# Optimization experiments

Hardware: AMD Instinct MI355X
Metric: run time of the kernel (lower is better)

## Reference

```python
import jax, jax.numpy as jnp
import numpy as np

B, V, T, F, H = 32, 16, 64, 64, 512
NBINS = 36  # 360 / delta (delta_cog = delta_rb = 10)
OUT = 4     # output_size


def setup_inputs() -> dict:
    key = jax.random.key(0)
    ks = jax.random.split(key, 12)
    s = 1.0 / np.sqrt(H)
    return {
        'sequence': jax.random.normal(ks[0], (B, V, T, F), jnp.float32),
        'dist_matrix': jax.random.uniform(ks[1], (B, V, T, V), jnp.float32),
        'rb_matrix': jax.random.randint(ks[2], (B, V, T, V), 0, NBINS).astype(jnp.int32),
        'cog_matrix': jax.random.randint(ks[3], (B, V, T, V), 0, NBINS).astype(jnp.int32),
        'seq_mask': jnp.ones((B, V, T), jnp.float32),
        'maxval': jax.random.uniform(ks[4], (B, F), jnp.float32) + 1.0,
        'minval': jax.random.uniform(ks[5], (B, F), jnp.float32),
        # per-vessel LSTMCell params (PyTorch gate order i,f,g,o stacked along 4H)
        'W_ih': jax.random.normal(ks[6], (V, 4 * H, F), jnp.float32) * s,
        'W_hh': jax.random.normal(ks[7], (V, 4 * H, H), jnp.float32) * s,
        'b_ih': jnp.zeros((V, 4 * H), jnp.float32),
        'b_hh': jnp.zeros((V, 4 * H), jnp.float32),
        # hardwired attention domain table [360/delta_cog, 360/delta_rb]
        'domain': jax.random.normal(ks[8], (NBINS, NBINS), jnp.float32),
        # per-vessel softAttention linear (2H -> H)
        'soft_W': jax.random.normal(ks[9], (V, H, 2 * H), jnp.float32) * s,
        'soft_b': jnp.zeros((V, H), jnp.float32),
        # shared output linear (H -> F)
        'out_W': jax.random.normal(ks[10], (F, H), jnp.float32) * s,
        'out_b': jnp.zeros((F,), jnp.float32),
    }


def _forward(sequence, dist_matrix, rb_matrix, cog_matrix, seq_mask, maxval, minval,
             W_ih, W_hh, b_ih, b_hh, domain, soft_W, soft_b, out_W, out_b):
    B_, V_, T_, F_ = sequence.shape
    H_ = W_hh.shape[-1]

    def hardwired(h, r, d, m, cg):
        # h: [B,V,H]; r,d,cg: [B,V,V]; m: [B,V]
        mul1 = m[:, :, None] * m[:, None, :]
        mul2 = domain[cg, r]
        w = jax.nn.relu(mul2 - d) * mul1
        w = w / jax.lax.stop_gradient(jnp.max(w))  # torch: weights /= weights.data.max()
        return jnp.einsum('bvw,bwh->bvh', w, h)

    def lstm_step(x, h, c):
        # vectorized over V independent LSTMCells
        g = (jnp.einsum('bvf,vgf->bvg', x, W_ih)
             + jnp.einsum('bvh,vgh->bvg', h, W_hh) + b_ih + b_hh)
        i, f, gg, o = jnp.split(g, 4, axis=-1)
        c_new = jax.nn.sigmoid(f) * c + jax.nn.sigmoid(i) * jnp.tanh(gg)
        h_new = jax.nn.sigmoid(o) * jnp.tanh(c_new)
        return h_new, c_new

    h0 = jnp.zeros((B_, V_, H_), sequence.dtype)
    c0 = jnp.zeros((B_, V_, H_), sequence.dtype)
    xs = (jnp.moveaxis(sequence, 2, 0), jnp.moveaxis(rb_matrix, 2, 0),
          jnp.moveaxis(dist_matrix, 2, 0), jnp.moveaxis(seq_mask, 2, 0),
          jnp.moveaxis(cog_matrix, 2, 0))

    def enc_step(carry, xt):
        h, c = carry
        x, r, d, m, cg = xt
        wh = hardwired(h, r, d, m, cg)
        h, c = lstm_step(x, wh, c)
        return (h, c), h

    (h, c), enc = jax.lax.scan(enc_step, (h0, c0), xs)
    enc = jnp.moveaxis(enc, 0, 2)  # encodedInput [B,V,T,H]

    # decoder, prediction step i=0 (prediction_length=1)
    wh = hardwired(h, rb_matrix[:, :, -1], dist_matrix[:, :, -1],
                   seq_mask[:, :, -1], cog_matrix[:, :, -1])
    # get_previous_sequence: denormalize under no_grad
    prev = jax.lax.stop_gradient(
        sequence[:, :, -1] * (maxval - minval)[:, None, :] + minval[:, None, :])
    h, c = lstm_step(prev, wh, c)

    # per-vessel softAttention
    score = jnp.einsum('bvth,bvh->bvt', enc, h)
    alpha = jax.nn.softmax(score * seq_mask, axis=-1)
    ctx = jnp.einsum('bvt,bvth->bvh', alpha, enc)
    # faithful to torch.stack((ctx, h)).view(B, 2H) memory-reinterpret per vessel
    z = jnp.moveaxis(jnp.stack([ctx, h], axis=0), 2, 0).reshape(V_, B_, 2 * H_)
    h = jnp.moveaxis(
        jnp.tanh(jnp.einsum('vbk,vhk->vbh', z, soft_W) + soft_b[:, None, :]), 0, 1)

    out = jax.nn.relu(jnp.einsum('bvh,fh->bvf', h, out_W) + out_b)
    return out[:, :, None, :OUT]  # [B, V, prediction_length=1, output_size]


def reference(sequence, dist_matrix, rb_matrix, cog_matrix, seq_mask, maxval, minval,
              W_ih, W_hh, b_ih, b_hh, domain, soft_W, soft_b, out_W, out_b,
              maxVessels=V):
    return _forward(sequence, dist_matrix, rb_matrix, cog_matrix, seq_mask,
                    maxval, minval, W_ih, W_hh, b_ih, b_hh, domain,
                    soft_W, soft_b, out_W, out_b)
```

## Files before the change

kernel.cpp:

```cpp
#include <hip/hip_runtime.h>
#include <math.h>

#define B 32
#define V 16
#define T 64
#define F 64
#define H 512
#define NB 36
#define G4H 2048

typedef unsigned short u16;
typedef unsigned long long ull;
typedef __attribute__((ext_vector_type(8))) short bf16x8;
typedef __attribute__((ext_vector_type(4))) float f32x4;

#define OFF_H0     0
#define OFF_H1     262144
#define OFF_C      524288
#define OFF_CNT    786432
#define OFF_WALL   819200
#define OFF_CTX    819200
#define OFF_HSOFT  1081344
#define OFF_WMAX   1343488
#define OFF_WHSTG  1343552
#define OFF_SEQSTG 1605696
#define OFF_WSTG   2670656
#define OFF_ENC    12107840

#define WHP 262144
#define WLDS_BYTES 147456

__device__ __forceinline__ float sigmoidf_(float x) { return 1.0f / (1.0f + __expf(-x)); }

__device__ __forceinline__ u16 f2bf(float f) {
    union { float f; unsigned u; } x; x.f = f;
    unsigned r = x.u + 0x7FFF + ((x.u >> 16) & 1);
    return (u16)(r >> 16);
}
__device__ __forceinline__ float bf2f(u16 u) {
    union { unsigned i; float f; } x; x.i = ((unsigned)u) << 16;
    return x.f;
}
__device__ __forceinline__ f32x4 mfma16(bf16x8 a, bf16x8 b, f32x4 c) {
    return __builtin_amdgcn_mfma_f32_16x16x32_bf16(a, b, c, 0, 0, 0);
}
__device__ __forceinline__ bf16x8 mk_bf16x8(ull lo, ull hi) {
    union { ull u[2]; bf16x8 v; } x; x.u[0] = lo; x.u[1] = hi; return x.v;
}
__device__ __forceinline__ bf16x8 mk_bf16x8q(uint4 q) {
    union { uint4 q; bf16x8 v; } x; x.q = q; return x.v;
}

__device__ __forceinline__ ull ld_agent(const ull* p) {
    return __hip_atomic_load((ull*)p, __ATOMIC_RELAXED, __HIP_MEMORY_SCOPE_AGENT);
}
__device__ __forceinline__ void st_agent(ull* p, ull x) {
    __hip_atomic_store(p, x, __ATOMIC_RELAXED, __HIP_MEMORY_SCOPE_AGENT);
}
__device__ __forceinline__ void st_agent_f(float* p, float x) {
    __hip_atomic_store(p, x, __ATOMIC_RELAXED, __HIP_MEMORY_SCOPE_AGENT);
}
__device__ __forceinline__ void st_agent_u32(unsigned* p, unsigned x) {
    __hip_atomic_store(p, x, __ATOMIC_RELAXED, __HIP_MEMORY_SCOPE_AGENT);
}
__device__ __forceinline__ unsigned ld_agent_u32(const unsigned* p) {
    return __hip_atomic_load((unsigned*)p, __ATOMIC_RELAXED, __HIP_MEMORY_SCOPE_AGENT);
}

#define NZB 3200
#define NHW 64
#define NWC 256
#define NSS 1040
__global__ __launch_bounds__(256) void k_prep(
    float* __restrict__ ws,
    const float* __restrict__ dist, const int* __restrict__ rb,
    const int* __restrict__ cog, const float* __restrict__ mask,
    const float* __restrict__ domain, float* __restrict__ w_all,
    float* __restrict__ wmax_all,
    const float* __restrict__ W_ih, const float* __restrict__ W_hh,
    u16* __restrict__ Wstg,
    const float* __restrict__ seq, const float* __restrict__ maxval,
    const float* __restrict__ minval, u16* __restrict__ seqstg) {
    __shared__ float red[256];
    __shared__ float tile[128 * 36];
    int bid = blockIdx.x;
    int tid = threadIdx.x;

    if (bid < NZB) {
        ws[bid * 256 + tid] = 0.0f;
        return;
    }
    if (bid < NZB + NHW) {
        int t = bid - NZB;
        float lmax = 0.0f;
        for (int idx = tid; idx < B * V * V; idx += 256) {
            int b = idx >> 8;
            int rem = idx & 255;
            int i = rem >> 4, j = rem & 15;
            int base = ((b * V + i) * T + t) * V + j;
            float val = domain[cog[base] * NB + rb[base]] - dist[base];
            val = val > 0.0f ? val : 0.0f;
            val *= mask[(b * V + i) * T + t] * mask[(b * V + j) * T + t];
            w_all[t * (B * V * V) + idx] = val;
            lmax = fmaxf(lmax, val);
        }
        red[tid] = lmax;
        __syncthreads();
        for (int s = 128; s > 0; s >>= 1) {
            if (tid < s) red[tid] = fmaxf(red[tid], red[tid + s]);
            __syncthreads();
        }
        if (tid == 0) wmax_all[t] = red[0];
        return;
    }
    if (bid < NZB + NHW + NWC) {
        int idx = bid - (NZB + NHW);
        int v = idx >> 4, hk = idx & 15;
        int lr = tid >> 1, half = tid & 1;
        int lg = lr >> 5, rloc = lr & 31;
        int srcrow = v * G4H + lg * 512 + hk * 32 + rloc;
        for (int ks = 0; ks < 18; ++ks) {
            const float* srcp = (ks < 2)
                ? &W_ih[srcrow * F + ks * 32 + half * 16]
                : &W_hh[srcrow * H + (ks * 32 - 64) + half * 16];
            float4 x0 = *(const float4*)srcp;
            float4 x1 = *(const float4*)(srcp + 4);
            float4 x2 = *(const float4*)(srcp + 8);
            float4 x3 = *(const float4*)(srcp + 12);
            __syncthreads();
            float* dst = &tile[lr * 36 + half * 16];
            *(float4*)(dst + 0) = x0;
            *(float4*)(dst + 4) = x1;
            *(float4*)(dst + 8) = x2;
            *(float4*)(dst + 12) = x3;
            __syncthreads();
#pragma unroll
            for (int s = 0; s < 2; ++s) {
                int slot = tid + s * 256;
                int nt = slot >> 6, lane = slot & 63;
                int g = nt >> 1, hh = nt & 1;
                int ldsrow = g * 32 + hh * 16 + (lane & 15);
                int kloc = (lane >> 4) << 3;
                float4 y0 = *(const float4*)&tile[ldsrow * 36 + kloc];
                float4 y1 = *(const float4*)&tile[ldsrow * 36 + kloc + 4];
                union { u16 u[8]; uint4 q; } pk;
                pk.u[0] = f2bf(y0.x); pk.u[1] = f2bf(y0.y);
                pk.u[2] = f2bf(y0.z); pk.u[3] = f2bf(y0.w);
                pk.u[4] = f2bf(y1.x); pk.u[5] = f2bf(y1.y);
                pk.u[6] = f2bf(y1.z); pk.u[7] = f2bf(y1.w);
                *(uint4*)&Wstg[(size_t)((((v * 16 + hk) * 18 + ks) * 8 + nt) * 64 + lane) * 8] = pk.q;
            }
        }
        return;
    }
    {
        int idx = bid - (NZB + NHW + NWC);
        int v = idx / 65, t = idx % 65;
        int mt = tid >> 7, ks = (tid >> 6) & 1, lane = tid & 63;
        int b = mt * 16 + (lane & 15);
        int f = ks * 32 + ((lane >> 4) << 3);
        union { u16 u[8]; uint4 q; } pk;
        if (t < T) {
            const float* sp = &seq[((b * V + v) * T + t) * F + f];
            float4 x0 = *(const float4*)sp, x1 = *(const float4*)(sp + 4);
            pk.u[0] = f2bf(x0.x); pk.u[1] = f2bf(x0.y); pk.u[2] = f2bf(x0.z); pk.u[3] = f2bf(x0.w);
            pk.u[4] = f2bf(x1.x); pk.u[5] = f2bf(x1.y); pk.u[6] = f2bf(x1.z); pk.u[7] = f2bf(x1.w);
        } else {
            const float* sp = &seq[((b * V + v) * T + (T - 1)) * F + f];
            float4 x0 = *(const float4*)sp, x1 = *(const float4*)(sp + 4);
            float4 mx0 = *(const float4*)&maxval[b * F + f], mx1 = *(const float4*)&maxval[b * F + f + 4];
            float4 mn0 = *(const float4*)&minval[b * F + f], mn1 = *(const float4*)&minval[b * F + f + 4];
            pk.u[0] = f2bf(x0.x * (mx0.x - mn0.x) + mn0.x);
            pk.u[1] = f2bf(x0.y * (mx0.y - mn0.y) + mn0.y);
            pk.u[2] = f2bf(x0.z * (mx0.z - mn0.z) + mn0.z);
            pk.u[3] = f2bf(x0.w * (mx0.w - mn0.w) + mn0.w);
            pk.u[4] = f2bf(x1.x * (mx1.x - mn1.x) + mn1.x);
            pk.u[5] = f2bf(x1.y * (mx1.y - mn1.y) + mn1.y);
            pk.u[6] = f2bf(x1.z * (mx1.z - mn1.z) + mn1.z);
            pk.u[7] = f2bf(x1.w * (mx1.w - mn1.w) + mn1.w);
        }
        *(uint4*)&seqstg[(((size_t)(t * 16 + v)) * 4 + mt * 2 + ks) * 512 + lane * 8] = pk.q;
    }
}

__global__ __launch_bounds__(256) void k_recur(
    const u16* __restrict__ seqstg, const u16* __restrict__ Wstg,
    const float* __restrict__ w_all, const float* __restrict__ wmax_all,
    const float* __restrict__ b_ih, const float* __restrict__ b_hh,
    float* __restrict__ h0buf, float* __restrict__ h1buf,
    float* __restrict__ c, u16* __restrict__ enc, u16* __restrict__ whstg,
    unsigned* __restrict__ bar) {
    extern __shared__ u16 Wlds[];

    int bid = blockIdx.x;
    int v = bid & 15, hk = bid >> 4;
    int tid = threadIdx.x;

    {
        const uint4* wsrc = (const uint4*)(Wstg + (size_t)((v * 16 + hk) * 18) * 4096);
        uint4* wdst = (uint4*)Wlds;
        for (int i = tid; i < 9216; i += 256) wdst[i] = wsrc[i];
    }

    int lane = tid & 63, wvi = tid >> 6;
    int mtw = wvi & 1, hh = wvi >> 1;
    int col = hk * 32 + hh * 16 + (lane & 15);
    int q4 = (lane >> 4) << 2;
    float bi = b_ih[v * G4H + col] + b_hh[v * G4H + col];
    float bf_ = b_ih[v * G4H + H + col] + b_hh[v * G4H + H + col];
    float bg_ = b_ih[v * G4H + 2 * H + col] + b_hh[v * G4H + 2 * H + col];
    float bo = b_ih[v * G4H + 3 * H + col] + b_hh[v * G4H + 3 * H + col];

    unsigned* aslot = bar + (v * 16 + hk) * 16;
    unsigned* bslot = bar + (256 + hk * 16 + v) * 16;
    unsigned* apoll = bar + (v * 16 + (tid & 15)) * 16;
    unsigned* bpoll = bar + (256 + hk * 16 + (tid & 15)) * 16;

    int a_b = tid >> 3;
    int a_cq = tid & 7;
    const int wh_idx = ((((v * 2 + (a_b >> 4)) * 16 + hk) * 64 +
                         (((a_cq >> 1) << 4) + (a_b & 15))) * 8 + (a_cq & 1) * 4);

    __syncthreads();

    for (int t = 0; t <= T; ++t) {
        int par = t & 1;
        int tm = t < T ? t : (T - 1);
        const float* hin = (t & 1) ? h0buf : h1buf;
        float* hout = (t & 1) ? h1buf : h0buf;

        uint4 s0 = *(const uint4*)&seqstg[(((size_t)(t * 16 + v)) * 4 + mtw * 2 + 0) * 512 + lane * 8];
        uint4 s1 = *(const uint4*)&seqstg[(((size_t)(t * 16 + v)) * 4 + mtw * 2 + 1) * 512 + lane * 8];
        float inv = 1.0f / wmax_all[tm];
        const float* wrow = &w_all[(size_t)tm * (B * V * V) + (a_b * V + v) * V];
        float4 wr0 = *(const float4*)(wrow);
        float4 wr1 = *(const float4*)(wrow + 4);
        float4 wr2 = *(const float4*)(wrow + 8);
        float4 wr3 = *(const float4*)(wrow + 12);
        float cprev[4];
#pragma unroll
        for (int r = 0; r < 4; ++r)
            cprev[r] = c[((mtw * 16 + q4 + r) * V + v) * H + col];

        f32x4 acc[4];
        acc[0][0] = bi;  acc[0][1] = bi;  acc[0][2] = bi;  acc[0][3] = bi;
        acc[1][0] = bf_; acc[1][1] = bf_; acc[1][2] = bf_; acc[1][3] = bf_;
        acc[2][0] = bg_; acc[2][1] = bg_; acc[2][2] = bg_; acc[2][3] = bg_;
        acc[3][0] = bo;  acc[3][1] = bo;  acc[3][2] = bo;  acc[3][3] = bo;
        {
            bf16x8 a0f = mk_bf16x8q(s0);
            bf16x8 a1f = mk_bf16x8q(s1);
#pragma unroll
            for (int g = 0; g < 4; ++g)
                acc[g] = mfma16(a0f, *(const bf16x8*)&Wlds[(0 * 8 + (g * 2 + hh)) * 512 + lane * 8], acc[g]);
#pragma unroll
            for (int g = 0; g < 4; ++g)
                acc[g] = mfma16(a1f, *(const bf16x8*)&Wlds[(1 * 8 + (g * 2 + hh)) * 512 + lane * 8], acc[g]);
        }

        if (t > 0) {
            if (tid < 16) {
                while (ld_agent_u32(bpoll) < (unsigned)t) __builtin_amdgcn_s_sleep(1);
            }
            __syncthreads();
        }

        {
            const ull* hb = (const ull*)&hin[(a_b * V) * H + hk * 32 + a_cq * 4];
            float a0 = 0.f, a1 = 0.f, a2 = 0.f, a3 = 0.f;
            const float wj[16] = {wr0.x, wr0.y, wr0.z, wr0.w, wr1.x, wr1.y, wr1.z, wr1.w,
                                  wr2.x, wr2.y, wr2.z, wr2.w, wr3.x, wr3.y, wr3.z, wr3.w};
#pragma unroll
            for (int j = 0; j < 16; ++j) {
                ull lo = ld_agent(hb + (size_t)j * (H / 2));
                ull hi = ld_agent(hb + (size_t)j * (H / 2) + 1);
                union { ull u; float f[2]; } u0, u1;
                u0.u = lo; u1.u = hi;
                a0 = fmaf(wj[j], u0.f[0], a0);
                a1 = fmaf(wj[j], u0.f[1], a1);
                a2 = fmaf(wj[j], u1.f[0], a2);
                a3 = fmaf(wj[j], u1.f[1], a3);
            }
            union { u16 u[4]; ull q; } pk;
            pk.u[0] = f2bf(a0 * inv); pk.u[1] = f2bf(a1 * inv);
            pk.u[2] = f2bf(a2 * inv); pk.u[3] = f2bf(a3 * inv);
            st_agent((ull*)&whstg[par * WHP + wh_idx], pk.q);
        }
        __syncthreads();
        if (tid == 0) st_agent_u32(aslot, (unsigned)(t + 1));

        if (tid < 16) {
            while (ld_agent_u32(apoll) < (unsigned)(t + 1)) __builtin_amdgcn_s_sleep(1);
        }
        __syncthreads();

        bf16x8 afr[16];
#pragma unroll
        for (int ksw = 0; ksw < 16; ++ksw) {
            const ull* src = (const ull*)&whstg[par * WHP + (((v * 2 + mtw) * 16 + ksw) * 64 + lane) * 8];
            ull lo = ld_agent(src), hi = ld_agent(src + 1);
            afr[ksw] = mk_bf16x8(lo, hi);
        }
#pragma unroll
        for (int ks = 0; ks < 16; ++ks) {
#pragma unroll
            for (int g = 0; g < 4; ++g) {
                bf16x8 wfr = *(const bf16x8*)&Wlds[((ks + 2) * 8 + (g * 2 + hh)) * 512 + lane * 8];
                acc[g] = mfma16(afr[ks], wfr, acc[g]);
            }
        }

        float cnv[4], hnv[4];
#pragma unroll
        for (int r = 0; r < 4; ++r) {
            float gi = acc[0][r];
            float gf = acc[1][r];
            float gg = acc[2][r];
            float go = acc[3][r];
            cnv[r] = sigmoidf_(gf) * cprev[r] + sigmoidf_(gi) * tanhf(gg);
            hnv[r] = sigmoidf_(go) * tanhf(cnv[r]);
            int b = mtw * 16 + q4 + r;
            st_agent_f(&hout[(b * V + v) * H + col], hnv[r]);
        }
        if (t < T) {
            __syncthreads();
            if (tid == 0) st_agent_u32(bslot, (unsigned)(t + 1));
        }

#pragma unroll
        for (int r = 0; r < 4; ++r) {
            int b = mtw * 16 + q4 + r;
            c[(b * V + v) * H + col] = cnv[r];
            if (t < T) enc[((size_t)(b * V + v) * T + t) * H + col] = f2bf(hnv[r]);
        }
    }
}

__global__ __launch_bounds__(256) void k_tail(
    const u16* __restrict__ enc, const float* __restrict__ hfin,
    const float* __restrict__ mask, const float* __restrict__ soft_W,
    const float* __restrict__ soft_b, const float* __restrict__ out_W,
    const float* __restrict__ out_b, float* __restrict__ ctx,
    float* __restrict__ hsoft, float* __restrict__ out,
    unsigned* __restrict__ bar) {
    __shared__ float hs[H];
    __shared__ float scal[2 * T];
    __shared__ float sA[32][36];
    __shared__ float sW2[32][36];

    int bid = blockIdx.x;
    int tid = threadIdx.x;
    int lane = tid & 63, wvi = tid >> 6;

    for (int u = 0; u < 2; ++u) {
        int ab = (bid >> 4) + u * 16;
        int av = bid & 15;
        const u16* encb = enc + ((size_t)(ab * V + av) * T) * H;
        {
            float2 q = *(const float2*)(hfin + (ab * V + av) * H + tid * 2);
            hs[tid * 2] = q.x; hs[tid * 2 + 1] = q.y;
        }
        __syncthreads();
        for (int tt = wvi; tt < T; tt += 4) {
            uint4 x = *(const uint4*)(encb + tt * H + lane * 8);
            union { uint4 q; u16 s[8]; } e; e.q = x;
            const float* hq = &hs[lane * 8];
            float p = bf2f(e.s[0]) * hq[0] + bf2f(e.s[1]) * hq[1]
                    + bf2f(e.s[2]) * hq[2] + bf2f(e.s[3]) * hq[3]
                    + bf2f(e.s[4]) * hq[4] + bf2f(e.s[5]) * hq[5]
                    + bf2f(e.s[6]) * hq[6] + bf2f(e.s[7]) * hq[7];
            for (int off = 32; off; off >>= 1) p += __shfl_down(p, off, 64);
            if (lane == 0) scal[tt] = p;
        }
        __syncthreads();
        if (tid < 64) {
            float m_t = mask[(ab * V + av) * T + tid];
            float s = scal[tid] * m_t;
            float mx = s;
            for (int off = 32; off; off >>= 1) mx = fmaxf(mx, __shfl_xor(mx, off, 64));
            float e = __expf(s - mx);
            float sum = e;
            for (int off = 32; off; off >>= 1) sum += __shfl_xor(sum, off, 64);
            scal[T + tid] = e / sum;
        }
        __syncthreads();
        if (tid < 128) {
            float a0 = 0.f, a1 = 0.f, a2 = 0.f, a3 = 0.f;
            for (int tt = 0; tt < T; ++tt) {
                ull x = *(const ull*)(encb + tt * H + tid * 4);
                union { ull u; u16 s[4]; } q; q.u = x;
                float al = scal[T + tt];
                a0 = fmaf(al, bf2f(q.s[0]), a0);
                a1 = fmaf(al, bf2f(q.s[1]), a1);
                a2 = fmaf(al, bf2f(q.s[2]), a2);
                a3 = fmaf(al, bf2f(q.s[3]), a3);
            }
            float* cp = ctx + (ab * V + av) * H + tid * 4;
            union { float f[2]; ull u; } q0, q1;
            q0.f[0] = a0; q0.f[1] = a1; q1.f[0] = a2; q1.f[1] = a3;
            st_agent((ull*)cp, q0.u);
            st_agent((ull*)cp + 1, q1.u);
        }
        __syncthreads();
    }
    __syncthreads();
    if (tid == 0) st_agent_u32(bar + (768 + bid) * 16, 1u);

    {
        int sv = bid & 15;
        int h0 = (bid >> 4) * 32;
        if (tid < 16) {
            const unsigned* cs = bar + (768 + tid * 16 + sv) * 16;
            while (ld_agent_u32(cs) < 1u) __builtin_amdgcn_s_sleep(1);
        }
        __syncthreads();

        int cg = tid & 31, rg = tid >> 5;
        float* sAf = &sA[0][0];
        float* sWf = &sW2[0][0];
        float accs[4] = {0.f, 0.f, 0.f, 0.f};
        int arow = tid >> 3, akq = tid & 7;
        float4 areg, wreg;
        {
            int k = akq * 4;
            const float* src = (arow < 16) ? ctx : hfin;
            int bsrc = 2 * (arow & 15) + (k >= H ? 1 : 0);
            const float* sp = &src[(bsrc * V + sv) * H + (k & (H - 1))];
            ull l0 = ld_agent((const ull*)sp), l1 = ld_agent((const ull*)sp + 1);
            union { ull u[2]; float4 f; } q; q.u[0] = l0; q.u[1] = l1;
            areg = q.f;
            wreg = *(const float4*)&soft_W[(sv * H + h0 + arow) * (2 * H) + k];
        }
        for (int kc = 0; kc < 2 * H; kc += 32) {
            __syncthreads();
            *(float4*)&sAf[arow * 36 + akq * 4] = areg;
            *(float4*)&sWf[arow * 36 + akq * 4] = wreg;
            __syncthreads();
            if (kc + 32 < 2 * H) {
                int k = kc + 32 + akq * 4;
                const float* src = (arow < 16) ? ctx : hfin;
                int bsrc = 2 * (arow & 15) + (k >= H ? 1 : 0);
                const float* sp = &src[(bsrc * V + sv) * H + (k & (H - 1))];
                ull l0 = ld_agent((const ull*)sp), l1 = ld_agent((const ull*)sp + 1);
                union { ull u[2]; float4 f; } q; q.u[0] = l0; q.u[1] = l1;
                areg = q.f;
                wreg = *(const float4*)&soft_W[(sv * H + h0 + arow) * (2 * H) + kc + 32 + akq * 4];
            }
#pragma unroll
            for (int k4 = 0; k4 < 8; ++k4) {
                float4 wv = *(const float4*)&sWf[cg * 36 + k4 * 4];
                float4 a0 = *(const float4*)&sAf[(rg * 4 + 0) * 36 + k4 * 4];
                float4 a1 = *(const float4*)&sAf[(rg * 4 + 1) * 36 + k4 * 4];
                float4 a2 = *(const float4*)&sAf[(rg * 4 + 2) * 36 + k4 * 4];
                float4 a3 = *(const float4*)&sAf[(rg * 4 + 3) * 36 + k4 * 4];
                accs[0] += a0.x * wv.x + a0.y * wv.y + a0.z * wv.z + a0.w * wv.w;
                accs[1] += a1.x * wv.x + a1.y * wv.y + a1.z * wv.z + a1.w * wv.w;
                accs[2] += a2.x * wv.x + a2.y * wv.y + a2.z * wv.z + a2.w * wv.w;
                accs[3] += a3.x * wv.x + a3.y * wv.y + a3.z * wv.z + a3.w * wv.w;
            }
        }
        float bb = soft_b[sv * H + h0 + cg];
#pragma unroll
        for (int r = 0; r < 4; ++r) {
            int row = rg * 4 + r;
            st_agent_f(&hsoft[(row * V + sv) * H + h0 + cg], tanhf(accs[r] + bb));
        }
    }
    __syncthreads();
    if (tid == 0) st_agent_u32(bar + (1024 + bid) * 16, 1u);

    {
        int ov = bid & 15;
        if (tid < 16) {
            const unsigned* ss = bar + (1024 + tid * 16 + ov) * 16;
            while (ld_agent_u32(ss) < 1u) __builtin_amdgcn_s_sleep(1);
        }
        __syncthreads();
        if (wvi < 2) {
            int ob = (bid >> 4) + wvi * 16;
            const float* hbp = hsoft + (ob * V + ov) * H + lane * 8;
            ull q0 = ld_agent((const ull*)hbp);
            ull q1 = ld_agent((const ull*)hbp + 1);
            ull q2 = ld_agent((const ull*)hbp + 2);
            ull q3 = ld_agent((const ull*)hbp + 3);
            union { ull u[4]; float f[8]; } hv;
            hv.u[0] = q0; hv.u[1] = q1; hv.u[2] = q2; hv.u[3] = q3;
            float p[4] = {0.f, 0.f, 0.f, 0.f};
#pragma unroll
            for (int o = 0; o < 4; ++o) {
                const float* wp = &out_W[o * H + lane * 8];
#pragma unroll
                for (int j = 0; j < 8; ++j) p[o] += hv.f[j] * wp[j];
            }
#pragma unroll
            for (int o = 0; o < 4; ++o) {
                float s = p[o];
                for (int off = 32; off; off >>= 1) s += __shfl_down(s, off, 64);
                if (lane == 0) {
                    float val = s + out_b[o];
                    out[(ob * V + ov) * 4 + o] = val > 0.0f ? val : 0.0f;
                }
            }
        }
    }
}

extern "C" void kernel_launch(void* const* d_in, const int* in_sizes, int n_in,
                              void* d_out, int out_size, void* d_ws, size_t ws_size,
                              hipStream_t stream) {
    const float* seq = (const float*)d_in[0];
    const float* dist = (const float*)d_in[1];
    const int* rb = (const int*)d_in[2];
    const int* cog = (const int*)d_in[3];
    const float* mask = (const float*)d_in[4];
    const float* maxval = (const float*)d_in[5];
    const float* minval = (const float*)d_in[6];
    const float* W_ih = (const float*)d_in[7];
    const float* W_hh = (const float*)d_in[8];
    const float* b_ih = (const float*)d_in[9];
    const float* b_hh = (const float*)d_in[10];
    const float* domain = (const float*)d_in[11];
    const float* soft_W = (const float*)d_in[12];
    const float* soft_b = (const float*)d_in[13];
    const float* out_W = (const float*)d_in[14];
    const float* out_b = (const float*)d_in[15];

    float* ws = (float*)d_ws;
    float* h0buf = ws + OFF_H0;
    float* h1buf = ws + OFF_H1;
    float* c = ws + OFF_C;
    unsigned* bar = (unsigned*)(ws + OFF_CNT);
    float* w_all = ws + OFF_WALL;
    float* ctx = ws + OFF_CTX;
    float* hsoft = ws + OFF_HSOFT;
    float* wmax_all = ws + OFF_WMAX;
    u16* whstg = (u16*)(ws + OFF_WHSTG);
    u16* seqstg = (u16*)(ws + OFF_SEQSTG);
    u16* Wstg = (u16*)(ws + OFF_WSTG);
    u16* enc = (u16*)(ws + OFF_ENC);

    (void)hipFuncSetAttribute((const void*)k_recur,
                              hipFuncAttributeMaxDynamicSharedMemorySize, WLDS_BYTES);

    k_prep<<<NZB + NHW + NWC + NSS, 256, 0, stream>>>(
        ws, dist, rb, cog, mask, domain, w_all, wmax_all,
        W_ih, W_hh, Wstg, seq, maxval, minval, seqstg);

    k_recur<<<256, 256, WLDS_BYTES, stream>>>(seqstg, Wstg, w_all, wmax_all,
                                              b_ih, b_hh, h0buf, h1buf, c, enc,
                                              whstg, bar);

    k_tail<<<256, 256, 0, stream>>>(enc, h0buf, mask, soft_W, soft_b,
                                    out_W, out_b, ctx, hsoft,
                                    (float*)d_out, bar);
}
```

Measured before the change: 710.0 us.

## Convert LSTM weights to bf16 directly into LDS inside the recurrent kernel

The prep kernel no longer converts W_ih/W_hh into a global bf16 staging buffer. Each recurrent block now reads fp32 weights from global memory, converts them to bf16 and writes them straight into its LDS tile. Zeroing of h1 and c moves from the prep kernel into the recurrent blocks, so the prep kernel only zeros the counter region. The barrier counter is shifted by one so every block publishes readiness after its own init. This removes a global write-and-reload round trip and most of the zeroing blocks. The cost is slower uncoalesced fp32 loads at the start of the recurrent kernel, and the cross-block barrier protocol changes.

```diff
diff --git a/kernel.cpp b/kernel.cpp
--- a/kernel.cpp
+++ b/kernel.cpp
@@ -24,7 +24,6 @@
 #define OFF_WMAX   1343488
 #define OFF_WHSTG  1343552
 #define OFF_SEQSTG 1605696
-#define OFF_WSTG   2670656
 #define OFF_ENC    12107840
 
 #define WHP 262144
@@ -67,9 +66,8 @@
     return __hip_atomic_load((unsigned*)p, __ATOMIC_RELAXED, __HIP_MEMORY_SCOPE_AGENT);
 }
 
-#define NZB 3200
+#define NZB 80
 #define NHW 64
-#define NWC 256
 #define NSS 1040
 __global__ __launch_bounds__(256) void k_prep(
     float* __restrict__ ws,
@@ -77,17 +75,14 @@
     const int* __restrict__ cog, const float* __restrict__ mask,
     const float* __restrict__ domain, float* __restrict__ w_all,
     float* __restrict__ wmax_all,
-    const float* __restrict__ W_ih, const float* __restrict__ W_hh,
-    u16* __restrict__ Wstg,
     const float* __restrict__ seq, const float* __restrict__ maxval,
     const float* __restrict__ minval, u16* __restrict__ seqstg) {
     __shared__ float red[256];
-    __shared__ float tile[128 * 36];
     int bid = blockIdx.x;
     int tid = threadIdx.x;
 
     if (bid < NZB) {
-        ws[bid * 256 + tid] = 0.0f;
+        ws[OFF_CNT + bid * 256 + tid] = 0.0f;
         return;
     }
     if (bid < NZB + NHW) {
@@ -113,48 +108,8 @@
         if (tid == 0) wmax_all[t] = red[0];
         return;
     }
-    if (bid < NZB + NHW + NWC) {
+    {
         int idx = bid - (NZB + NHW);
-        int v = idx >> 4, hk = idx & 15;
-        int lr = tid >> 1, half = tid & 1;
-        int lg = lr >> 5, rloc = lr & 31;
-        int srcrow = v * G4H + lg * 512 + hk * 32 + rloc;
-        for (int ks = 0; ks < 18; ++ks) {
-            const float* srcp = (ks < 2)
-                ? &W_ih[srcrow * F + ks * 32 + half * 16]
-                : &W_hh[srcrow * H + (ks * 32 - 64) + half * 16];
-            float4 x0 = *(const float4*)srcp;
-            float4 x1 = *(const float4*)(srcp + 4);
-            float4 x2 = *(const float4*)(srcp + 8);
-            float4 x3 = *(const float4*)(srcp + 12);
-            __syncthreads();
-            float* dst = &tile[lr * 36 + half * 16];
-            *(float4*)(dst + 0) = x0;
-            *(float4*)(dst + 4) = x1;
-            *(float4*)(dst + 8) = x2;
-            *(float4*)(dst + 12) = x3;
-            __syncthreads();
-#pragma unroll
-            for (int s = 0; s < 2; ++s) {
-                int slot = tid + s * 256;
-                int nt = slot >> 6, lane = slot & 63;
-                int g = nt >> 1, hh = nt & 1;
-                int ldsrow = g * 32 + hh * 16 + (lane & 15);
-                int kloc = (lane >> 4) << 3;
-                float4 y0 = *(const float4*)&tile[ldsrow * 36 + kloc];
-                float4 y1 = *(const float4*)&tile[ldsrow * 36 + kloc + 4];
-                union { u16 u[8]; uint4 q; } pk;
-                pk.u[0] = f2bf(y0.x); pk.u[1] = f2bf(y0.y);
-                pk.u[2] = f2bf(y0.z); pk.u[3] = f2bf(y0.w);
-                pk.u[4] = f2bf(y1.x); pk.u[5] = f2bf(y1.y);
-                pk.u[6] = f2bf(y1.z); pk.u[7] = f2bf(y1.w);
-                *(uint4*)&Wstg[(size_t)((((v * 16 + hk) * 18 + ks) * 8 + nt) * 64 + lane) * 8] = pk.q;
-            }
-        }
-        return;
-    }
-    {
-        int idx = bid - (NZB + NHW + NWC);
         int v = idx / 65, t = idx % 65;
         int mt = tid >> 7, ks = (tid >> 6) & 1, lane = tid & 63;
         int b = mt * 16 + (lane & 15);
@@ -184,7 +139,8 @@
 }
 
 __global__ __launch_bounds__(256) void k_recur(
-    const u16* __restrict__ seqstg, const u16* __restrict__ Wstg,
+    const u16* __restrict__ seqstg,
+    const float* __restrict__ W_ih, const float* __restrict__ W_hh,
     const float* __restrict__ w_all, const float* __restrict__ wmax_all,
     const float* __restrict__ b_ih, const float* __restrict__ b_hh,
     float* __restrict__ h0buf, float* __restrict__ h1buf,
@@ -196,16 +152,45 @@
     int v = bid & 15, hk = bid >> 4;
     int tid = threadIdx.x;
 
-    {
-        const uint4* wsrc = (const uint4*)(Wstg + (size_t)((v * 16 + hk) * 18) * 4096);
-        uint4* wdst = (uint4*)Wlds;
-        for (int i = tid; i < 9216; i += 256) wdst[i] = wsrc[i];
-    }
-
     int lane = tid & 63, wvi = tid >> 6;
     int mtw = wvi & 1, hh = wvi >> 1;
     int col = hk * 32 + hh * 16 + (lane & 15);
     int q4 = (lane >> 4) << 2;
+
+    {
+#pragma unroll 2
+        for (int s = 0; s < 2; ++s) {
+            int slot = tid + s * 256;
+            int nt = slot >> 6, ln = slot & 63;
+            int g = nt >> 1, hh2 = nt & 1;
+            int row = v * G4H + g * H + hk * 32 + hh2 * 16 + (ln & 15);
+            int kq = (ln >> 4) << 3;
+            for (int ks = 0; ks < 18; ++ks) {
+                int k = ks * 32 + kq;
+                const float* src = (k < F) ? &W_ih[(size_t)row * F + k]
+                                           : &W_hh[(size_t)row * H + (k - F)];
+                float4 x0 = *(const float4*)src;
+                float4 x1 = *(const float4*)(src + 4);
+                union { u16 u[8]; uint4 q; } pk;
+                pk.u[0] = f2bf(x0.x); pk.u[1] = f2bf(x0.y);
+                pk.u[2] = f2bf(x0.z); pk.u[3] = f2bf(x0.w);
+                pk.u[4] = f2bf(x1.x); pk.u[5] = f2bf(x1.y);
+                pk.u[6] = f2bf(x1.z); pk.u[7] = f2bf(x1.w);
+                *(uint4*)&Wlds[(ks * 8 + nt) * 512 + ln * 8] = pk.q;
+            }
+        }
+    }
+
+    {
+        int zb = tid >> 3, zq = tid & 7;
+        ull* zp = (ull*)&h1buf[(zb * V + v) * H + hk * 32 + zq * 4];
+        st_agent(zp, 0ull);
+        st_agent(zp + 1, 0ull);
+#pragma unroll
+        for (int r = 0; r < 4; ++r)
+            c[((mtw * 16 + q4 + r) * V + v) * H + col] = 0.0f;
+    }
+
     float bi = b_ih[v * G4H + col] + b_hh[v * G4H + col];
     float bf_ = b_ih[v * G4H + H + col] + b_hh[v * G4H + H + col];
     float bg_ = b_ih[v * G4H + 2 * H + col] + b_hh[v * G4H + 2 * H + col];
@@ -222,6 +207,7 @@
                          (((a_cq >> 1) << 4) + (a_b & 15))) * 8 + (a_cq & 1) * 4);
 
     __syncthreads();
+    if (tid == 0) st_agent_u32(bslot, 1u);
 
     for (int t = 0; t <= T; ++t) {
         int par = t & 1;
@@ -258,12 +244,10 @@
                 acc[g] = mfma16(a1f, *(const bf16x8*)&Wlds[(1 * 8 + (g * 2 + hh)) * 512 + lane * 8], acc[g]);
         }
 
-        if (t > 0) {
-            if (tid < 16) {
-                while (ld_agent_u32(bpoll) < (unsigned)t) __builtin_amdgcn_s_sleep(1);
-            }
-            __syncthreads();
-        }
+        if (tid < 16) {
+            while (ld_agent_u32(bpoll) < (unsigned)(t + 1)) __builtin_amdgcn_s_sleep(1);
+        }
+        __syncthreads();
 
         {
             const ull* hb = (const ull*)&hin[(a_b * V) * H + hk * 32 + a_cq * 4];
@@ -324,7 +308,7 @@
         }
         if (t < T) {
             __syncthreads();
-            if (tid == 0) st_agent_u32(bslot, (unsigned)(t + 1));
+            if (tid == 0) st_agent_u32(bslot, (unsigned)(t + 2));
         }
 
 #pragma unroll
@@ -536,19 +520,18 @@
     float* wmax_all = ws + OFF_WMAX;
     u16* whstg = (u16*)(ws + OFF_WHSTG);
     u16* seqstg = (u16*)(ws + OFF_SEQSTG);
-    u16* Wstg = (u16*)(ws + OFF_WSTG);
     u16* enc = (u16*)(ws + OFF_ENC);
 
     (void)hipFuncSetAttribute((const void*)k_recur,
                               hipFuncAttributeMaxDynamicSharedMemorySize, WLDS_BYTES);
 
-    k_prep<<<NZB + NHW + NWC + NSS, 256, 0, stream>>>(
+    k_prep<<<NZB + NHW + NSS, 256, 0, stream>>>(
         ws, dist, rb, cog, mask, domain, w_all, wmax_all,
-        W_ih, W_hh, Wstg, seq, maxval, minval, seqstg);
-
-    k_recur<<<256, 256, WLDS_BYTES, stream>>>(seqstg, Wstg, w_all, wmax_all,
-                                              b_ih, b_hh, h0buf, h1buf, c, enc,
-                                              whstg, bar);
+        seq, maxval, minval, seqstg);
+
+    k_recur<<<256, 256, WLDS_BYTES, stream>>>(seqstg, W_ih, W_hh, w_all,
+                                              wmax_all, b_ih, b_hh, h0buf,
+                                              h1buf, c, enc, whstg, bar);
 
     k_tail<<<256, 256, 0, stream>>>(enc, h0buf, mask, soft_W, soft_b,
                                     out_W, out_b, ctx, hsoft,
```

Measured after the change: 697.3 us (median of 2 runs). Within noise of the previous version (-1.8%).
